# Kernel optimization log

Measured on AMD Instinct MI355X. Metric: run time of the kernel, lower is better.

Reference implementation:

```python
import jax, jax.numpy as jnp
import numpy as np

N_NODES = 100000


def _sage_conv(x, src, dst, W_l, W_r, b):
    # mean aggregation of neighbor features over incoming edges (src -> dst)
    msgs = x[src]                                            # [E, d] gather
    agg = jax.ops.segment_sum(msgs, dst, num_segments=N_NODES)
    deg = jax.ops.segment_sum(jnp.ones_like(dst, dtype=x.dtype), dst,
                              num_segments=N_NODES)
    mean = agg / jnp.maximum(deg, 1.0)[:, None]              # [N, d]
    # PyG SAGEConv: lin_l(aggr) + lin_r(x); bias lives in lin_l
    return mean @ W_l + x @ W_r + b


def setup_inputs() -> dict:
    key = jax.random.key(0)
    k = jax.random.split(key, 8)
    d_in, d_h, E = 128, 128, 1600000
    scale_in = 1.0 / np.sqrt(d_in)
    scale_h = 1.0 / np.sqrt(d_h)
    return {
        "x": jax.random.normal(k[0], (N_NODES, d_in), dtype=jnp.float32),
        "edge_index": jax.random.randint(k[1], (2, E), 0, N_NODES, dtype=jnp.int64),
        "W_l0": jax.random.uniform(k[2], (d_in, d_h), jnp.float32, -scale_in, scale_in),
        "W_r0": jax.random.uniform(k[3], (d_in, d_h), jnp.float32, -scale_in, scale_in),
        "b0": jnp.zeros((d_h,), jnp.float32),
        "W_l1": jax.random.uniform(k[4], (d_h, d_h), jnp.float32, -scale_h, scale_h),
        "W_r1": jax.random.uniform(k[5], (d_h, d_h), jnp.float32, -scale_h, scale_h),
        "b1": jnp.zeros((d_h,), jnp.float32),
    }


def reference(x, edge_index, W_l0, W_r0, b0, W_l1, W_r1, b1):
    src, dst = edge_index[0], edge_index[1]
    h = _sage_conv(x, src, dst, W_l0, W_r0, b0)
    h = jax.nn.relu(h)  # dropout p=0.0 / eval mode -> identity
    h = _sage_conv(h, src, dst, W_l1, W_r1, b1)
    return h
```

## Files before the change

kernel.cpp:

```cpp
#include <hip/hip_runtime.h>


using bf16x8 = __attribute__((ext_vector_type(8))) __bf16;
using f32x4  = __attribute__((ext_vector_type(4))) float;
using f32x2  = __attribute__((ext_vector_type(2))) float;

__device__ __forceinline__ unsigned short f2bf(float f) {
    __bf16 b = (__bf16)f;
    return __builtin_bit_cast(unsigned short, b);
}
__device__ __forceinline__ unsigned pk2(float a, float b) {
    return (unsigned)f2bf(a) | ((unsigned)f2bf(b) << 16);
}

__device__ __forceinline__ int exscan1024(int v, int* wsum, int t) {
    int lane = t & 63, w = t >> 6;
    int x = v;
#pragma unroll
    for (int s = 1; s < 64; s <<= 1) {
        int y = __shfl_up(x, s);
        if (lane >= s) x += y;
    }
    if (lane == 63) wsum[w] = x;
    __syncthreads();
    if (w == 0) {
        int ws = (lane < 16) ? wsum[lane] : 0;
#pragma unroll
        for (int s = 1; s < 16; s <<= 1) {
            int y = __shfl_up(ws, s);
            if (lane >= s) ws += y;
        }
        if (lane < 16) wsum[lane] = ws;
    }
    __syncthreads();
    int base = (w > 0) ? wsum[w - 1] : 0;
    return base + x - v;
}


__global__ __launch_bounds__(256) void k_prep(
    const float4* __restrict__ x, uint4* __restrict__ xb8, int nvec, int ncvt,
    const float* __restrict__ W0, const float* __restrict__ W1,
    const float* __restrict__ W2, const float* __restrict__ W3,
    unsigned short* __restrict__ wsw, int ncvtw,
    const int* __restrict__ dst, int E, int* __restrict__ ghist, int nb, int nhist)
{
    __shared__ int lh[800];
    const int b = blockIdx.x;
    if (b < ncvt) {
        int i = b * 256 + threadIdx.x;
        if (i >= nvec) return;
        float4 a = x[2 * i], c = x[2 * i + 1];
        uint4 o;
        o.x = pk2(a.x, a.y);
        o.y = pk2(a.z, a.w);
        o.z = pk2(c.x, c.y);
        o.w = pk2(c.z, c.w);
        xb8[i] = o;
    } else if (b < ncvt + ncvtw) {
        int id = (b - ncvt) * 256 + threadIdx.x;
        int m = id >> 14, r = id & 16383;
        int c = r >> 7, k = r & 127;
        const float* W = (m == 0) ? W0 : (m == 1) ? W1 : (m == 2) ? W2 : W3;
        wsw[m * 16384 + c * 128 + (k ^ ((c & 7) << 3))] = f2bf(W[k * 128 + c]);
    } else {
        int hb = b - ncvt - ncvtw;
        for (int i = threadIdx.x; i < nb; i += 256) lh[i] = 0;
        __syncthreads();
        for (int e = hb * 256 + threadIdx.x; e < E; e += nhist * 256)
            atomicAdd(&lh[dst[e] >> 7], 1);
        __syncthreads();
        for (int i = threadIdx.x; i < nb; i += 256)
            if (lh[i]) atomicAdd(&ghist[i], lh[i]);
    }
}


__global__ __launch_bounds__(1024) void k_binscan(const int* __restrict__ ghist,
                                                  int* __restrict__ gbase,
                                                  int* __restrict__ gcur,
                                                  int* __restrict__ row_start,
                                                  int nb, int n, int E)
{
    __shared__ int wsum[16];
    int t = threadIdx.x;
    int v = (t < nb) ? ghist[t] : 0;
    int excl = exscan1024(v, wsum, t);
    if (t < nb) { gbase[t] = excl; gcur[t] = excl; }
    if (t == 0) { gbase[nb] = E; row_start[n] = E; }
}


#define SC_CHUNK 8192

__global__ __launch_bounds__(1024) void k_binscatter(const int* __restrict__ src,
                                                     const int* __restrict__ dst, int E,
                                                     int* __restrict__ gcur,
                                                     unsigned* __restrict__ binned, int nb)
{
    __shared__ int lh[800];
    __shared__ int lbase[800];
    __shared__ int gb[800];
    __shared__ int wsum[16];
    __shared__ unsigned long long staged[SC_CHUNK];
    int t = threadIdx.x;
    int e0 = blockIdx.x * SC_CHUNK;
    if (e0 >= E) return;
    int ecnt = E - e0; if (ecnt > SC_CHUNK) ecnt = SC_CHUNK;

    for (int i = t; i < nb; i += 1024) lh[i] = 0;
    __syncthreads();
    for (int i = t; i < ecnt; i += 1024)
        atomicAdd(&lh[dst[e0 + i] >> 7], 1);
    __syncthreads();
    int v = (t < nb) ? lh[t] : 0;
    int excl = exscan1024(v, wsum, t);
    if (t < nb) {
        lbase[t] = excl;
        gb[t] = v ? atomicAdd(&gcur[t], v) : 0;
        lh[t] = excl;
    }
    __syncthreads();
    for (int i = t; i < ecnt; i += 1024) {
        int d = dst[e0 + i], s = src[e0 + i];
        int b = d >> 7;
        int rank = atomicAdd(&lh[b], 1);
        unsigned pack = ((unsigned)s << 7) | (unsigned)(d & 127);
        unsigned gaddr = (unsigned)gb[b] + (unsigned)(rank - lbase[b]);
        staged[rank] = ((unsigned long long)gaddr << 32) | pack;
    }
    __syncthreads();
    for (int i = t; i < ecnt; i += 1024) {
        unsigned long long w = staged[i];
        binned[(unsigned)(w >> 32)] = (unsigned)w;
    }
}


#define BS_STAGE 8192

__global__ __launch_bounds__(256) void k_bucketsort(
    const unsigned* __restrict__ binned,
    const int* __restrict__ gbase,
    int* __restrict__ csr,
    int* __restrict__ row_start,
    float* __restrict__ inv_deg,
    int n)
{
    __shared__ int cnt[128];
    __shared__ int cur[128];
    __shared__ int wsum[4];
    __shared__ unsigned stg[BS_STAGE];
    const int t = threadIdx.x;
    const int b = blockIdx.x;
    const int beg = gbase[b], end = gbase[b + 1];
    const int len = end - beg;

    if (t < 128) cnt[t] = 0;
    __syncthreads();
    for (int i = beg + t; i < end; i += 256)
        atomicAdd(&cnt[binned[i] & 127], 1);
    __syncthreads();
    int v = (t < 128) ? cnt[t] : 0;
    {
        int lane = t & 63, w = t >> 6;
        int x = v;
#pragma unroll
        for (int s = 1; s < 64; s <<= 1) {
            int y = __shfl_up(x, s);
            if (lane >= s) x += y;
        }
        if (lane == 63) wsum[w] = x;
        __syncthreads();
        int base = (w == 1) ? wsum[0] : (w == 2) ? wsum[0] + wsum[1]
                 : (w == 3) ? wsum[0] + wsum[1] + wsum[2] : 0;
        int excl = base + x - v;
        if (t < 128) {
            cur[t] = excl;
            int node = b * 128 + t;
            if (node < n) {
                row_start[node] = beg + excl;
                inv_deg[node] = 1.f / (float)max(v, 1);
            }
        }
    }
    __syncthreads();

    if (len <= BS_STAGE) {
        for (int i = beg + t; i < end; i += 256) {
            unsigned w = binned[i];
            int r = atomicAdd(&cur[w & 127], 1);
            stg[r] = w >> 7;
        }
        __syncthreads();
        for (int i = t; i < len; i += 256)
            csr[beg + i] = (int)stg[i];
    } else {
        for (int i = beg + t; i < end; i += 256) {
            unsigned w = binned[i];
            int r = atomicAdd(&cur[w & 127], 1);
            csr[beg + r] = (int)(w >> 7);
        }
    }
}


__device__ __forceinline__ f32x2 up2(unsigned x) {
    return (f32x2){__builtin_bit_cast(float, x << 16),
                   __builtin_bit_cast(float, x & 0xffff0000u)};
}
__device__ __forceinline__ void acc8(f32x2* a, uint4 v) {
    a[0] += up2(v.x);
    a[1] += up2(v.y);
    a[2] += up2(v.z);
    a[3] += up2(v.w);
}

__global__ __launch_bounds__(256) void k_agg(
    const unsigned short* __restrict__ feat,
    const int* __restrict__ csr,
    const int* __restrict__ row_start,
    const float* __restrict__ inv_deg,
    unsigned short* __restrict__ mean, int n)
{
    const int nodeA = blockIdx.x * 8 + (threadIdx.x >> 6) * 2;
    if (nodeA >= n) return;
    const bool two = (nodeA + 1 < n);
    const int lane = threadIdx.x & 63;
    const int q  = lane >> 4;
    const int cg = (lane & 15) << 3;

    const int begA = row_start[nodeA];
    const int endA = row_start[nodeA + 1];
    const int endB = two ? row_start[nodeA + 2] : endA;

    f32x2 aA[4], aB[4];
#pragma unroll
    for (int j = 0; j < 4; ++j) { aA[j] = (f32x2){0.f, 0.f}; aB[j] = (f32x2){0.f, 0.f}; }

    int iA = begA, iB = endA;
    while (iA < endA || iB < endB) {
        int cntA = endA - iA; cntA = cntA > 64 ? 64 : cntA;
        int cntB = endB - iB; cntB = cntB > 64 ? 64 : cntB;
        int idxA = 0, idxB = 0;
        if (cntA) idxA = csr[iA + (lane < cntA ? lane : cntA - 1)];
        if (cntB) idxB = csr[iB + (lane < cntB ? lane : cntB - 1)];
        const int cA = cntA > 0 ? cntA - 1 : 0;
        const int cB = cntB > 0 ? cntB - 1 : 0;
        const int mx = cntA > cntB ? cntA : cntB;
        for (int e = 0; e < mx; e += 16) {
            const bool dA = e < cntA, dB = e < cntB;
            uint4 vA0, vA1, vA2, vA3, vB0, vB1, vB2, vB3;
            int rA0 = e + q, rA1 = e + 4 + q, rA2 = e + 8 + q, rA3 = e + 12 + q;
            int rB0 = rA0, rB1 = rA1, rB2 = rA2, rB3 = rA3;
            if (dA) {
                int s0 = __shfl(idxA, rA0 < cA ? rA0 : cA);
                int s1 = __shfl(idxA, rA1 < cA ? rA1 : cA);
                int s2 = __shfl(idxA, rA2 < cA ? rA2 : cA);
                int s3 = __shfl(idxA, rA3 < cA ? rA3 : cA);
                vA0 = *(const uint4*)(feat + ((size_t)s0 << 7) + cg);
                vA1 = *(const uint4*)(feat + ((size_t)s1 << 7) + cg);
                vA2 = *(const uint4*)(feat + ((size_t)s2 << 7) + cg);
                vA3 = *(const uint4*)(feat + ((size_t)s3 << 7) + cg);
            }
            if (dB) {
                int s0 = __shfl(idxB, rB0 < cB ? rB0 : cB);
                int s1 = __shfl(idxB, rB1 < cB ? rB1 : cB);
                int s2 = __shfl(idxB, rB2 < cB ? rB2 : cB);
                int s3 = __shfl(idxB, rB3 < cB ? rB3 : cB);
                vB0 = *(const uint4*)(feat + ((size_t)s0 << 7) + cg);
                vB1 = *(const uint4*)(feat + ((size_t)s1 << 7) + cg);
                vB2 = *(const uint4*)(feat + ((size_t)s2 << 7) + cg);
                vB3 = *(const uint4*)(feat + ((size_t)s3 << 7) + cg);
            }
            if (dA) {
                if (rA0 < cntA) acc8(aA, vA0);
                if (rA1 < cntA) acc8(aA, vA1);
                if (rA2 < cntA) acc8(aA, vA2);
                if (rA3 < cntA) acc8(aA, vA3);
            }
            if (dB) {
                if (rB0 < cntB) acc8(aB, vB0);
                if (rB1 < cntB) acc8(aB, vB1);
                if (rB2 < cntB) acc8(aB, vB2);
                if (rB3 < cntB) acc8(aB, vB3);
            }
        }
        iA += cntA;
        iB += cntB;
    }

#pragma unroll
    for (int j = 0; j < 4; ++j) {
        aA[j].x += __shfl_xor(aA[j].x, 16);
        aA[j].x += __shfl_xor(aA[j].x, 32);
        aA[j].y += __shfl_xor(aA[j].y, 16);
        aA[j].y += __shfl_xor(aA[j].y, 32);
        aB[j].x += __shfl_xor(aB[j].x, 16);
        aB[j].x += __shfl_xor(aB[j].x, 32);
        aB[j].y += __shfl_xor(aB[j].y, 16);
        aB[j].y += __shfl_xor(aB[j].y, 32);
    }

    if (q == 0) {
        float w = inv_deg[nodeA];
        uint4 o;
        o.x = pk2(aA[0].x * w, aA[0].y * w);
        o.y = pk2(aA[1].x * w, aA[1].y * w);
        o.z = pk2(aA[2].x * w, aA[2].y * w);
        o.w = pk2(aA[3].x * w, aA[3].y * w);
        *(uint4*)(mean + (size_t)nodeA * 128 + cg) = o;
        if (two) {
            float w2 = inv_deg[nodeA + 1];
            uint4 p;
            p.x = pk2(aB[0].x * w2, aB[0].y * w2);
            p.y = pk2(aB[1].x * w2, aB[1].y * w2);
            p.z = pk2(aB[2].x * w2, aB[2].y * w2);
            p.w = pk2(aB[3].x * w2, aB[3].y * w2);
            *(uint4*)(mean + (size_t)(nodeA + 1) * 128 + cg) = p;
        }
    }
}


template<bool RELU, bool OUTF32>
__global__ __launch_bounds__(256) void k_gemm(
    const unsigned short* __restrict__ A1,
    const unsigned short* __restrict__ A2,
    const unsigned short* __restrict__ Wsw,
    const float* __restrict__ bias,
    void* __restrict__ outv,
    int nrows)
{
    __shared__ __align__(16) unsigned short Wt[2 * 128 * 128];
    {
        const uint4* wsrc = (const uint4*)Wsw;
        uint4* wdst = (uint4*)Wt;
#pragma unroll
        for (int i = 0; i < 16; ++i)
            wdst[threadIdx.x + 256 * i] = wsrc[threadIdx.x + 256 * i];
    }
    __syncthreads();

    const int lane = threadIdx.x & 63;
    const int wave = threadIdx.x >> 6;
    const int lr = lane & 15;
    const int lg = lane >> 4;
    const int row0 = blockIdx.x * 128 + wave * 32;
    const int sw = (lr & 7) << 3;

    f32x4 acc[2][8];
#pragma unroll
    for (int m = 0; m < 2; ++m)
#pragma unroll
        for (int nn = 0; nn < 8; ++nn) acc[m][nn] = (f32x4){0.f, 0.f, 0.f, 0.f};

#pragma unroll
    for (int ks = 0; ks < 4; ++ks) {
        const int k0 = ks * 32 + lg * 8;
        bf16x8 a1[2], a2[2];
#pragma unroll
        for (int m = 0; m < 2; ++m) {
            int r = row0 + m * 16 + lr;
            if (r >= nrows) r = nrows - 1;
            a1[m] = *reinterpret_cast<const bf16x8*>(A1 + (size_t)r * 128 + k0);
            a2[m] = *reinterpret_cast<const bf16x8*>(A2 + (size_t)r * 128 + k0);
        }
        const int kidx = k0 ^ sw;
#pragma unroll
        for (int nn = 0; nn < 8; ++nn) {
            const int c = nn * 16 + lr;
            bf16x8 b1 = *reinterpret_cast<const bf16x8*>(&Wt[c * 128 + kidx]);
            bf16x8 b2 = *reinterpret_cast<const bf16x8*>(&Wt[16384 + c * 128 + kidx]);
#pragma unroll
            for (int m = 0; m < 2; ++m) {
                acc[m][nn] = __builtin_amdgcn_mfma_f32_16x16x32_bf16(a1[m], b1, acc[m][nn], 0, 0, 0);
                acc[m][nn] = __builtin_amdgcn_mfma_f32_16x16x32_bf16(a2[m], b2, acc[m][nn], 0, 0, 0);
            }
        }
    }

    __syncthreads();

#pragma unroll
    for (int m = 0; m < 2; ++m) {
#pragma unroll
        for (int nn = 0; nn < 8; ++nn) {
            const int c = nn * 16 + lr;
            const float bv = bias[c];
#pragma unroll
            for (int i = 0; i < 4; ++i) {
                int r = row0 + m * 16 + lg * 4 + i;
                if (r < nrows) {
                    float v = acc[m][nn][i] + bv;
                    if (RELU) v = fmaxf(v, 0.f);
                    if (OUTF32)
                        ((float*)outv)[(size_t)r * 128 + c] = v;
                    else
                        ((unsigned short*)outv)[(size_t)r * 128 + c] = f2bf(v);
                }
            }
        }
    }
}


extern "C" void kernel_launch(void* const* d_in, const int* in_sizes, int n_in,
                              void* d_out, int out_size, void* d_ws, size_t ws_size,
                              hipStream_t stream)
{
    const float* x   = (const float*)d_in[0];
    const int*   ei  = (const int*)d_in[1];
    const float* Wl0 = (const float*)d_in[2];
    const float* Wr0 = (const float*)d_in[3];
    const float* b0  = (const float*)d_in[4];
    const float* Wl1 = (const float*)d_in[5];
    const float* Wr1 = (const float*)d_in[6];
    const float* b1  = (const float*)d_in[7];
    float* out = (float*)d_out;

    const int n = in_sizes[0] / 128;
    const int E = in_sizes[1] / 2;
    const int* src = ei;
    const int* dst = ei + E;
    const int nb = (n + 127) >> 7;

    char* ws = (char*)d_ws;
    size_t off = 0;
    auto alloc = [&](size_t sz) -> char* {
        char* p = ws + off;
        off += (sz + 1023) & ~(size_t)1023;
        return p;
    };
    unsigned short* xb     = (unsigned short*)alloc((size_t)n * 128 * 2);
    unsigned short* mean   = (unsigned short*)alloc((size_t)n * 128 * 2);
    unsigned*       binned = (unsigned*)      alloc((size_t)E * 4);
    int*            rs     = (int*)           alloc((size_t)(n + 1) * 4);
    float*          invd   = (float*)         alloc((size_t)n * 4);
    int*            ghist  = (int*)           alloc((size_t)nb * 4);
    int*            gbase  = (int*)           alloc((size_t)(nb + 1) * 4);
    int*            gcur   = (int*)           alloc((size_t)nb * 4);
    unsigned short* wsw    = (unsigned short*)alloc(4 * 16384 * 2);
    int* csr;
    if (off + (size_t)E * 4 <= ws_size) csr = (int*)alloc((size_t)E * 4);
    else                                csr = (int*)binned;
    if (ws_size < off) return;

    const int nvec  = n * 128 / 8;
    const int ncvt  = (nvec + 255) / 256;
    const int ncvtw = 256;
    const int nhist = 512;
    const int nsc   = (E + SC_CHUNK - 1) / SC_CHUNK;

    hipMemsetAsync(ghist, 0, (size_t)nb * sizeof(int), stream);
    hipLaunchKernelGGL(k_prep, dim3(ncvt + ncvtw + nhist), dim3(256), 0, stream,
                       (const float4*)x, (uint4*)xb, nvec, ncvt,
                       Wl0, Wr0, Wl1, Wr1, wsw, ncvtw,
                       dst, E, ghist, nb, nhist);
    hipLaunchKernelGGL(k_binscan,    dim3(1),    dim3(1024), 0, stream,
                       ghist, gbase, gcur, rs, nb, n, E);
    hipLaunchKernelGGL(k_binscatter, dim3(nsc),  dim3(1024), 0, stream,
                       src, dst, E, gcur, binned, nb);
    hipLaunchKernelGGL(k_bucketsort, dim3(nb),   dim3(256),  0, stream,
                       binned, gbase, csr, rs, invd, n);
    hipLaunchKernelGGL(k_agg,  dim3((n + 7) / 8), dim3(256), 0, stream,
                       xb, csr, rs, invd, mean, n);
    hipLaunchKernelGGL((k_gemm<true, false>), dim3(nb), dim3(256), 0, stream,
                       mean, xb, wsw, b0, (void*)xb, n);
    hipLaunchKernelGGL(k_agg,  dim3((n + 7) / 8), dim3(256), 0, stream,
                       xb, csr, rs, invd, mean, n);
    hipLaunchKernelGGL((k_gemm<false, true>), dim3(nb), dim3(256), 0, stream,
                       mean, xb, wsw + 2 * 16384, b1, (void*)out, n);
}
```

Measured before the change: 227.5 us.

## Split neighbor aggregation into two feature-half passes for cache locality

The aggregation kernel now processes only 64 of the 128 feature columns per launch, and it is launched twice per layer, once per half. Each wavefront gathers 8 neighbors per step with 8 lanes per row instead of 4 neighbors with 16 lanes. The gathered working set per pass is half the bf16 feature table, so it is more likely to stay in L2/MALL and cut DRAM traffic from random gathers. The cost is reading the CSR indices twice, two extra kernel launches, and one more shuffle stage in the reduction.

```diff
diff --git a/kernel.cpp b/kernel.cpp
--- a/kernel.cpp
+++ b/kernel.cpp
@@ -216,19 +216,20 @@
     a[3] += up2(v.w);
 }
 
-__global__ __launch_bounds__(256) void k_agg(
+__global__ __launch_bounds__(256) void k_aggh(
     const unsigned short* __restrict__ feat,
     const int* __restrict__ csr,
     const int* __restrict__ row_start,
     const float* __restrict__ inv_deg,
-    unsigned short* __restrict__ mean, int n)
+    unsigned short* __restrict__ mean, int n, int half)
 {
     const int nodeA = blockIdx.x * 8 + (threadIdx.x >> 6) * 2;
     if (nodeA >= n) return;
     const bool two = (nodeA + 1 < n);
     const int lane = threadIdx.x & 63;
-    const int q  = lane >> 4;
-    const int cg = (lane & 15) << 3;
+    const int o  = lane >> 3;
+    const int cg = (lane & 7) << 3;
+    const unsigned short* fp = feat + half * 64 + cg;
 
     const int begA = row_start[nodeA];
     const int endA = row_start[nodeA + 1];
@@ -248,43 +249,37 @@
         const int cA = cntA > 0 ? cntA - 1 : 0;
         const int cB = cntB > 0 ? cntB - 1 : 0;
         const int mx = cntA > cntB ? cntA : cntB;
-        for (int e = 0; e < mx; e += 16) {
-            const bool dA = e < cntA, dB = e < cntB;
+        for (int e = 0; e < mx; e += 32) {
             uint4 vA0, vA1, vA2, vA3, vB0, vB1, vB2, vB3;
-            int rA0 = e + q, rA1 = e + 4 + q, rA2 = e + 8 + q, rA3 = e + 12 + q;
-            int rB0 = rA0, rB1 = rA1, rB2 = rA2, rB3 = rA3;
-            if (dA) {
-                int s0 = __shfl(idxA, rA0 < cA ? rA0 : cA);
-                int s1 = __shfl(idxA, rA1 < cA ? rA1 : cA);
-                int s2 = __shfl(idxA, rA2 < cA ? rA2 : cA);
-                int s3 = __shfl(idxA, rA3 < cA ? rA3 : cA);
-                vA0 = *(const uint4*)(feat + ((size_t)s0 << 7) + cg);
-                vA1 = *(const uint4*)(feat + ((size_t)s1 << 7) + cg);
-                vA2 = *(const uint4*)(feat + ((size_t)s2 << 7) + cg);
-                vA3 = *(const uint4*)(feat + ((size_t)s3 << 7) + cg);
-            }
-            if (dB) {
-                int s0 = __shfl(idxB, rB0 < cB ? rB0 : cB);
-                int s1 = __shfl(idxB, rB1 < cB ? rB1 : cB);
-                int s2 = __shfl(idxB, rB2 < cB ? rB2 : cB);
-                int s3 = __shfl(idxB, rB3 < cB ? rB3 : cB);
-                vB0 = *(const uint4*)(feat + ((size_t)s0 << 7) + cg);
-                vB1 = *(const uint4*)(feat + ((size_t)s1 << 7) + cg);
-                vB2 = *(const uint4*)(feat + ((size_t)s2 << 7) + cg);
-                vB3 = *(const uint4*)(feat + ((size_t)s3 << 7) + cg);
-            }
-            if (dA) {
-                if (rA0 < cntA) acc8(aA, vA0);
-                if (rA1 < cntA) acc8(aA, vA1);
-                if (rA2 < cntA) acc8(aA, vA2);
-                if (rA3 < cntA) acc8(aA, vA3);
-            }
-            if (dB) {
-                if (rB0 < cntB) acc8(aB, vB0);
-                if (rB1 < cntB) acc8(aB, vB1);
-                if (rB2 < cntB) acc8(aB, vB2);
-                if (rB3 < cntB) acc8(aB, vB3);
-            }
+            const int r0 = e + o, r1 = e + 8 + o, r2 = e + 16 + o, r3 = e + 24 + o;
+            const bool iA0 = e < cntA, iA1 = e + 8 < cntA,
+                       iA2 = e + 16 < cntA, iA3 = e + 24 < cntA;
+            const bool iB0 = e < cntB, iB1 = e + 8 < cntB,
+                       iB2 = e + 16 < cntB, iB3 = e + 24 < cntB;
+            if (iA0) { int s = __shfl(idxA, r0 < cA ? r0 : cA);
+                       vA0 = *(const uint4*)(fp + ((size_t)s << 7)); }
+            if (iA1) { int s = __shfl(idxA, r1 < cA ? r1 : cA);
+                       vA1 = *(const uint4*)(fp + ((size_t)s << 7)); }
+            if (iA2) { int s = __shfl(idxA, r2 < cA ? r2 : cA);
+                       vA2 = *(const uint4*)(fp + ((size_t)s << 7)); }
+            if (iA3) { int s = __shfl(idxA, r3 < cA ? r3 : cA);
+                       vA3 = *(const uint4*)(fp + ((size_t)s << 7)); }
+            if (iB0) { int s = __shfl(idxB, r0 < cB ? r0 : cB);
+                       vB0 = *(const uint4*)(fp + ((size_t)s << 7)); }
+            if (iB1) { int s = __shfl(idxB, r1 < cB ? r1 : cB);
+                       vB1 = *(const uint4*)(fp + ((size_t)s << 7)); }
+            if (iB2) { int s = __shfl(idxB, r2 < cB ? r2 : cB);
+                       vB2 = *(const uint4*)(fp + ((size_t)s << 7)); }
+            if (iB3) { int s = __shfl(idxB, r3 < cB ? r3 : cB);
+                       vB3 = *(const uint4*)(fp + ((size_t)s << 7)); }
+            if (iA0 && r0 < cntA) acc8(aA, vA0);
+            if (iA1 && r1 < cntA) acc8(aA, vA1);
+            if (iA2 && r2 < cntA) acc8(aA, vA2);
+            if (iA3 && r3 < cntA) acc8(aA, vA3);
+            if (iB0 && r0 < cntB) acc8(aB, vB0);
+            if (iB1 && r1 < cntB) acc8(aB, vB1);
+            if (iB2 && r2 < cntB) acc8(aB, vB2);
+            if (iB3 && r3 < cntB) acc8(aB, vB3);
         }
         iA += cntA;
         iB += cntB;
@@ -292,24 +287,28 @@
 
 #pragma unroll
     for (int j = 0; j < 4; ++j) {
+        aA[j].x += __shfl_xor(aA[j].x, 8);
         aA[j].x += __shfl_xor(aA[j].x, 16);
         aA[j].x += __shfl_xor(aA[j].x, 32);
+        aA[j].y += __shfl_xor(aA[j].y, 8);
         aA[j].y += __shfl_xor(aA[j].y, 16);
         aA[j].y += __shfl_xor(aA[j].y, 32);
+        aB[j].x += __shfl_xor(aB[j].x, 8);
         aB[j].x += __shfl_xor(aB[j].x, 16);
         aB[j].x += __shfl_xor(aB[j].x, 32);
+        aB[j].y += __shfl_xor(aB[j].y, 8);
         aB[j].y += __shfl_xor(aB[j].y, 16);
         aB[j].y += __shfl_xor(aB[j].y, 32);
     }
 
-    if (q == 0) {
+    if (o == 0) {
         float w = inv_deg[nodeA];
-        uint4 o;
-        o.x = pk2(aA[0].x * w, aA[0].y * w);
-        o.y = pk2(aA[1].x * w, aA[1].y * w);
-        o.z = pk2(aA[2].x * w, aA[2].y * w);
-        o.w = pk2(aA[3].x * w, aA[3].y * w);
-        *(uint4*)(mean + (size_t)nodeA * 128 + cg) = o;
+        uint4 u;
+        u.x = pk2(aA[0].x * w, aA[0].y * w);
+        u.y = pk2(aA[1].x * w, aA[1].y * w);
+        u.z = pk2(aA[2].x * w, aA[2].y * w);
+        u.w = pk2(aA[3].x * w, aA[3].y * w);
+        *(uint4*)(mean + (size_t)nodeA * 128 + half * 64 + cg) = u;
         if (two) {
             float w2 = inv_deg[nodeA + 1];
             uint4 p;
@@ -317,7 +316,7 @@
             p.y = pk2(aB[1].x * w2, aB[1].y * w2);
             p.z = pk2(aB[2].x * w2, aB[2].y * w2);
             p.w = pk2(aB[3].x * w2, aB[3].y * w2);
-            *(uint4*)(mean + (size_t)(nodeA + 1) * 128 + cg) = p;
+            *(uint4*)(mean + (size_t)(nodeA + 1) * 128 + half * 64 + cg) = p;
         }
     }
 }
@@ -451,6 +450,7 @@
     const int ncvtw = 256;
     const int nhist = 512;
     const int nsc   = (E + SC_CHUNK - 1) / SC_CHUNK;
+    const int nagg  = (n + 7) / 8;
 
     hipMemsetAsync(ghist, 0, (size_t)nb * sizeof(int), stream);
     hipLaunchKernelGGL(k_prep, dim3(ncvt + ncvtw + nhist), dim3(256), 0, stream,
@@ -463,12 +463,16 @@
                        src, dst, E, gcur, binned, nb);
     hipLaunchKernelGGL(k_bucketsort, dim3(nb),   dim3(256),  0, stream,
                        binned, gbase, csr, rs, invd, n);
-    hipLaunchKernelGGL(k_agg,  dim3((n + 7) / 8), dim3(256), 0, stream,
-                       xb, csr, rs, invd, mean, n);
+    hipLaunchKernelGGL(k_aggh, dim3(nagg), dim3(256), 0, stream,
+                       xb, csr, rs, invd, mean, n, 0);
+    hipLaunchKernelGGL(k_aggh, dim3(nagg), dim3(256), 0, stream,
+                       xb, csr, rs, invd, mean, n, 1);
     hipLaunchKernelGGL((k_gemm<true, false>), dim3(nb), dim3(256), 0, stream,
                        mean, xb, wsw, b0, (void*)xb, n);
-    hipLaunchKernelGGL(k_agg,  dim3((n + 7) / 8), dim3(256), 0, stream,
-                       xb, csr, rs, invd, mean, n);
+    hipLaunchKernelGGL(k_aggh, dim3(nagg), dim3(256), 0, stream,
+                       xb, csr, rs, invd, mean, n, 0);
+    hipLaunchKernelGGL(k_aggh, dim3(nagg), dim3(256), 0, stream,
+                       xb, csr, rs, invd, mean, n, 1);
     hipLaunchKernelGGL((k_gemm<false, true>), dim3(nb), dim3(256), 0, stream,
                        mean, xb, wsw + 2 * 16384, b1, (void*)out, n);
 }
```

After: 301.2 us. +32.4%, slower.

## Fold bin scan into histogram via last-block-wins; simplify aggregation to one node per wave

Applied to the files above, without the earlier changes.

The separate single-block scan kernel is removed. The last histogram block to finish, detected with an atomic counter stored after the histogram, now computes the exclusive scan of bin counts, which saves one kernel launch and its serialization gap. The aggregation kernel is also reduced from two interleaved nodes per wave to one node per wave. Each lane now loads CSR indices directly instead of broadcasting them through shuffles. This lowers register pressure and control complexity but loses the two-node overlap of gather latency.

```diff
diff --git a/kernel.cpp b/kernel.cpp
--- a/kernel.cpp
+++ b/kernel.cpp
@@ -43,7 +43,9 @@
     const float* __restrict__ W0, const float* __restrict__ W1,
     const float* __restrict__ W2, const float* __restrict__ W3,
     unsigned short* __restrict__ wsw, int ncvtw,
-    const int* __restrict__ dst, int E, int* __restrict__ ghist, int nb, int nhist)
+    const int* __restrict__ dst, int E, int* __restrict__ ghist, int nb, int nhist,
+    int* __restrict__ gbase, int* __restrict__ gcur,
+    int* __restrict__ row_start, int n)
 {
     __shared__ int lh[800];
     const int b = blockIdx.x;
@@ -72,22 +74,43 @@
         __syncthreads();
         for (int i = threadIdx.x; i < nb; i += 256)
             if (lh[i]) atomicAdd(&ghist[i], lh[i]);
-    }
-}
-
-
-__global__ __launch_bounds__(1024) void k_binscan(const int* __restrict__ ghist,
-                                                  int* __restrict__ gbase,
-                                                  int* __restrict__ gcur,
-                                                  int* __restrict__ row_start,
-                                                  int nb, int n, int E)
-{
-    __shared__ int wsum[16];
-    int t = threadIdx.x;
-    int v = (t < nb) ? ghist[t] : 0;
-    int excl = exscan1024(v, wsum, t);
-    if (t < nb) { gbase[t] = excl; gcur[t] = excl; }
-    if (t == 0) { gbase[nb] = E; row_start[n] = E; }
+
+        __shared__ int winflag;
+        __shared__ int swsum[4];
+        if (threadIdx.x == 0) {
+            __threadfence();
+            winflag = (atomicAdd(&ghist[nb], 1) == nhist - 1) ? 1 : 0;
+        }
+        __syncthreads();
+        if (!winflag) return;
+        __threadfence();
+
+        const int t = threadIdx.x, lane = t & 63, w = t >> 6;
+        const int i0 = t * 4;
+        int v0 = (i0 + 0 < nb) ? __hip_atomic_load(&ghist[i0 + 0], __ATOMIC_RELAXED, __HIP_MEMORY_SCOPE_AGENT) : 0;
+        int v1 = (i0 + 1 < nb) ? __hip_atomic_load(&ghist[i0 + 1], __ATOMIC_RELAXED, __HIP_MEMORY_SCOPE_AGENT) : 0;
+        int v2 = (i0 + 2 < nb) ? __hip_atomic_load(&ghist[i0 + 2], __ATOMIC_RELAXED, __HIP_MEMORY_SCOPE_AGENT) : 0;
+        int v3 = (i0 + 3 < nb) ? __hip_atomic_load(&ghist[i0 + 3], __ATOMIC_RELAXED, __HIP_MEMORY_SCOPE_AGENT) : 0;
+        int s = v0 + v1 + v2 + v3;
+        int xx = s;
+#pragma unroll
+        for (int sh = 1; sh < 64; sh <<= 1) {
+            int y = __shfl_up(xx, sh);
+            if (lane >= sh) xx += y;
+        }
+        if (lane == 63) swsum[w] = xx;
+        __syncthreads();
+        int base = 0;
+        if (w > 0) base += swsum[0];
+        if (w > 1) base += swsum[1];
+        if (w > 2) base += swsum[2];
+        int run = base + xx - s;
+        if (i0 + 0 < nb) { gbase[i0 + 0] = run; gcur[i0 + 0] = run; } run += v0;
+        if (i0 + 1 < nb) { gbase[i0 + 1] = run; gcur[i0 + 1] = run; } run += v1;
+        if (i0 + 2 < nb) { gbase[i0 + 2] = run; gcur[i0 + 2] = run; } run += v2;
+        if (i0 + 3 < nb) { gbase[i0 + 3] = run; gcur[i0 + 3] = run; }
+        if (t == 0) { gbase[nb] = E; row_start[n] = E; }
+    }
 }
 
 
@@ -223,102 +246,57 @@
     const float* __restrict__ inv_deg,
     unsigned short* __restrict__ mean, int n)
 {
-    const int nodeA = blockIdx.x * 8 + (threadIdx.x >> 6) * 2;
-    if (nodeA >= n) return;
-    const bool two = (nodeA + 1 < n);
+    const int node = blockIdx.x * 4 + (threadIdx.x >> 6);
+    if (node >= n) return;
     const int lane = threadIdx.x & 63;
     const int q  = lane >> 4;
     const int cg = (lane & 15) << 3;
-
-    const int begA = row_start[nodeA];
-    const int endA = row_start[nodeA + 1];
-    const int endB = two ? row_start[nodeA + 2] : endA;
-
-    f32x2 aA[4], aB[4];
-#pragma unroll
-    for (int j = 0; j < 4; ++j) { aA[j] = (f32x2){0.f, 0.f}; aB[j] = (f32x2){0.f, 0.f}; }
-
-    int iA = begA, iB = endA;
-    while (iA < endA || iB < endB) {
-        int cntA = endA - iA; cntA = cntA > 64 ? 64 : cntA;
-        int cntB = endB - iB; cntB = cntB > 64 ? 64 : cntB;
-        int idxA = 0, idxB = 0;
-        if (cntA) idxA = csr[iA + (lane < cntA ? lane : cntA - 1)];
-        if (cntB) idxB = csr[iB + (lane < cntB ? lane : cntB - 1)];
-        const int cA = cntA > 0 ? cntA - 1 : 0;
-        const int cB = cntB > 0 ? cntB - 1 : 0;
-        const int mx = cntA > cntB ? cntA : cntB;
-        for (int e = 0; e < mx; e += 16) {
-            const bool dA = e < cntA, dB = e < cntB;
-            uint4 vA0, vA1, vA2, vA3, vB0, vB1, vB2, vB3;
-            int rA0 = e + q, rA1 = e + 4 + q, rA2 = e + 8 + q, rA3 = e + 12 + q;
-            int rB0 = rA0, rB1 = rA1, rB2 = rA2, rB3 = rA3;
-            if (dA) {
-                int s0 = __shfl(idxA, rA0 < cA ? rA0 : cA);
-                int s1 = __shfl(idxA, rA1 < cA ? rA1 : cA);
-                int s2 = __shfl(idxA, rA2 < cA ? rA2 : cA);
-                int s3 = __shfl(idxA, rA3 < cA ? rA3 : cA);
-                vA0 = *(const uint4*)(feat + ((size_t)s0 << 7) + cg);
-                vA1 = *(const uint4*)(feat + ((size_t)s1 << 7) + cg);
-                vA2 = *(const uint4*)(feat + ((size_t)s2 << 7) + cg);
-                vA3 = *(const uint4*)(feat + ((size_t)s3 << 7) + cg);
-            }
-            if (dB) {
-                int s0 = __shfl(idxB, rB0 < cB ? rB0 : cB);
-                int s1 = __shfl(idxB, rB1 < cB ? rB1 : cB);
-                int s2 = __shfl(idxB, rB2 < cB ? rB2 : cB);
-                int s3 = __shfl(idxB, rB3 < cB ? rB3 : cB);
-                vB0 = *(const uint4*)(feat + ((size_t)s0 << 7) + cg);
-                vB1 = *(const uint4*)(feat + ((size_t)s1 << 7) + cg);
-                vB2 = *(const uint4*)(feat + ((size_t)s2 << 7) + cg);
-                vB3 = *(const uint4*)(feat + ((size_t)s3 << 7) + cg);
-            }
-            if (dA) {
-                if (rA0 < cntA) acc8(aA, vA0);
-                if (rA1 < cntA) acc8(aA, vA1);
-                if (rA2 < cntA) acc8(aA, vA2);
-                if (rA3 < cntA) acc8(aA, vA3);
-            }
-            if (dB) {
-                if (rB0 < cntB) acc8(aB, vB0);
-                if (rB1 < cntB) acc8(aB, vB1);
-                if (rB2 < cntB) acc8(aB, vB2);
-                if (rB3 < cntB) acc8(aB, vB3);
-            }
-        }
-        iA += cntA;
-        iB += cntB;
+    const unsigned short* fp = feat + cg;
+    const int beg = row_start[node], end = row_start[node + 1];
+
+    f32x2 a[4];
+#pragma unroll
+    for (int j = 0; j < 4; ++j) a[j] = (f32x2){0.f, 0.f};
+
+    for (int i = beg; i < end; i += 64) {
+        int cnt = end - i; if (cnt > 64) cnt = 64;
+        const int lim = i + cnt - 1;
+        for (int e = 0; e < cnt; e += 16) {
+            int p0 = i + e + q;      p0 = p0 < lim ? p0 : lim;
+            int p1 = i + e + 4 + q;  p1 = p1 < lim ? p1 : lim;
+            int p2 = i + e + 8 + q;  p2 = p2 < lim ? p2 : lim;
+            int p3 = i + e + 12 + q; p3 = p3 < lim ? p3 : lim;
+            int s0 = csr[p0];
+            int s1 = csr[p1];
+            int s2 = csr[p2];
+            int s3 = csr[p3];
+            uint4 v0 = *(const uint4*)(fp + ((size_t)s0 << 7));
+            uint4 v1 = *(const uint4*)(fp + ((size_t)s1 << 7));
+            uint4 v2 = *(const uint4*)(fp + ((size_t)s2 << 7));
+            uint4 v3 = *(const uint4*)(fp + ((size_t)s3 << 7));
+            if (e + q      < cnt) acc8(a, v0);
+            if (e + 4 + q  < cnt) acc8(a, v1);
+            if (e + 8 + q  < cnt) acc8(a, v2);
+            if (e + 12 + q < cnt) acc8(a, v3);
+        }
     }
 
 #pragma unroll
     for (int j = 0; j < 4; ++j) {
-        aA[j].x += __shfl_xor(aA[j].x, 16);
-        aA[j].x += __shfl_xor(aA[j].x, 32);
-        aA[j].y += __shfl_xor(aA[j].y, 16);
-        aA[j].y += __shfl_xor(aA[j].y, 32);
-        aB[j].x += __shfl_xor(aB[j].x, 16);
-        aB[j].x += __shfl_xor(aB[j].x, 32);
-        aB[j].y += __shfl_xor(aB[j].y, 16);
-        aB[j].y += __shfl_xor(aB[j].y, 32);
+        a[j].x += __shfl_xor(a[j].x, 16);
+        a[j].x += __shfl_xor(a[j].x, 32);
+        a[j].y += __shfl_xor(a[j].y, 16);
+        a[j].y += __shfl_xor(a[j].y, 32);
     }
 
     if (q == 0) {
-        float w = inv_deg[nodeA];
+        float w = inv_deg[node];
         uint4 o;
-        o.x = pk2(aA[0].x * w, aA[0].y * w);
-        o.y = pk2(aA[1].x * w, aA[1].y * w);
-        o.z = pk2(aA[2].x * w, aA[2].y * w);
-        o.w = pk2(aA[3].x * w, aA[3].y * w);
-        *(uint4*)(mean + (size_t)nodeA * 128 + cg) = o;
-        if (two) {
-            float w2 = inv_deg[nodeA + 1];
-            uint4 p;
-            p.x = pk2(aB[0].x * w2, aB[0].y * w2);
-            p.y = pk2(aB[1].x * w2, aB[1].y * w2);
-            p.z = pk2(aB[2].x * w2, aB[2].y * w2);
-            p.w = pk2(aB[3].x * w2, aB[3].y * w2);
-            *(uint4*)(mean + (size_t)(nodeA + 1) * 128 + cg) = p;
-        }
+        o.x = pk2(a[0].x * w, a[0].y * w);
+        o.y = pk2(a[1].x * w, a[1].y * w);
+        o.z = pk2(a[2].x * w, a[2].y * w);
+        o.w = pk2(a[3].x * w, a[3].y * w);
+        *(uint4*)(mean + (size_t)node * 128 + cg) = o;
     }
 }
 
@@ -437,7 +415,7 @@
     unsigned*       binned = (unsigned*)      alloc((size_t)E * 4);
     int*            rs     = (int*)           alloc((size_t)(n + 1) * 4);
     float*          invd   = (float*)         alloc((size_t)n * 4);
-    int*            ghist  = (int*)           alloc((size_t)nb * 4);
+    int*            ghist  = (int*)           alloc((size_t)(nb + 1) * 4);
     int*            gbase  = (int*)           alloc((size_t)(nb + 1) * 4);
     int*            gcur   = (int*)           alloc((size_t)nb * 4);
     unsigned short* wsw    = (unsigned short*)alloc(4 * 16384 * 2);
@@ -452,22 +430,21 @@
     const int nhist = 512;
     const int nsc   = (E + SC_CHUNK - 1) / SC_CHUNK;
 
-    hipMemsetAsync(ghist, 0, (size_t)nb * sizeof(int), stream);
+    hipMemsetAsync(ghist, 0, (size_t)(nb + 1) * sizeof(int), stream);
     hipLaunchKernelGGL(k_prep, dim3(ncvt + ncvtw + nhist), dim3(256), 0, stream,
                        (const float4*)x, (uint4*)xb, nvec, ncvt,
                        Wl0, Wr0, Wl1, Wr1, wsw, ncvtw,
-                       dst, E, ghist, nb, nhist);
-    hipLaunchKernelGGL(k_binscan,    dim3(1),    dim3(1024), 0, stream,
-                       ghist, gbase, gcur, rs, nb, n, E);
+                       dst, E, ghist, nb, nhist,
+                       gbase, gcur, rs, n);
     hipLaunchKernelGGL(k_binscatter, dim3(nsc),  dim3(1024), 0, stream,
                        src, dst, E, gcur, binned, nb);
     hipLaunchKernelGGL(k_bucketsort, dim3(nb),   dim3(256),  0, stream,
                        binned, gbase, csr, rs, invd, n);
-    hipLaunchKernelGGL(k_agg,  dim3((n + 7) / 8), dim3(256), 0, stream,
+    hipLaunchKernelGGL(k_agg,  dim3((n + 3) / 4), dim3(256), 0, stream,
                        xb, csr, rs, invd, mean, n);
     hipLaunchKernelGGL((k_gemm<true, false>), dim3(nb), dim3(256), 0, stream,
                        mean, xb, wsw, b0, (void*)xb, n);
-    hipLaunchKernelGGL(k_agg,  dim3((n + 7) / 8), dim3(256), 0, stream,
+    hipLaunchKernelGGL(k_agg,  dim3((n + 3) / 4), dim3(256), 0, stream,
                        xb, csr, rs, invd, mean, n);
     hipLaunchKernelGGL((k_gemm<false, true>), dim3(nb), dim3(256), 0, stream,
                        mean, xb, wsw + 2 * 16384, b1, (void*)out, n);
```

Result: slower. 235.9 us (+3.7%).
